# Kernel optimization log

Hardware: AMD Instinct MI355X
Metric: run time of the kernel (lower is better)

Reference implementation:

```python
import jax, jax.numpy as jnp
import numpy as np

B, S, D = 1, 2048, 4096
NH, NKV, HD = 32, 8, 128
N_REP = NH // NKV
NEG = -1e9


def setup_inputs() -> dict:
    key = jax.random.key(0)
    ks = jax.random.split(key, 8)
    x = jax.random.normal(ks[0], (B, S, D), dtype=jnp.float32)
    # rotary freqs (theta=10000), shape [S, HD//2]
    inv = 1.0 / (10000.0 ** (jnp.arange(0, HD, 2, dtype=jnp.float32) / HD))
    ang = jnp.arange(S, dtype=jnp.float32)[:, None] * inv[None, :]
    freqs_cos, freqs_sin = jnp.cos(ang), jnp.sin(ang)
    # causal mask [1,1,S,S]
    row = jnp.arange(S)[:, None]
    col = jnp.arange(S)[None, :]
    mask = jnp.where(col <= row, 0.0, NEG).astype(jnp.float32)[None, None]
    input_indexes = jnp.arange(S, dtype=jnp.int64)
    cache_k = jnp.zeros((B, S, NKV, HD), dtype=jnp.float32)
    cache_v = jnp.zeros((B, S, NKV, HD), dtype=jnp.float32)
    sc = 0.02
    wq = jax.random.normal(ks[1], (NH * HD, D), dtype=jnp.float32) * sc
    wk = jax.random.normal(ks[2], (NKV * HD, D), dtype=jnp.float32) * sc
    wv = jax.random.normal(ks[3], (NKV * HD, D), dtype=jnp.float32) * sc
    wo = jax.random.normal(ks[4], (NH * HD, D), dtype=jnp.float32).T * sc
    return {"x": x, "freqs_cos": freqs_cos, "freqs_sin": freqs_sin, "mask": mask,
            "input_indexes": input_indexes, "cache_k": cache_k, "cache_v": cache_v,
            "wq": wq, "wk": wk, "wv": wv, "wo": wo}


def _rope(t, cos, sin):
    # t: [B,S,H,HD]; treat last dim as HD//2 complex pairs (even=real, odd=imag)
    tr = t.reshape(*t.shape[:-1], HD // 2, 2)
    xr, xi = tr[..., 0], tr[..., 1]
    c = cos[None, :, None, :]  # [1,S,1,HD//2]
    s = sin[None, :, None, :]
    outr = xr * c - xi * s
    outi = xr * s + xi * c
    return jnp.stack([outr, outi], axis=-1).reshape(t.shape)


def reference(x, freqs_cos, freqs_sin, mask, input_indexes, cache_k, cache_v, wq, wk, wv, wo):
    bsz, seqlen = x.shape[0], x.shape[-2]
    xq = (x @ wq.T).reshape(bsz, seqlen, NH, HD)
    xk = (x @ wk.T).reshape(bsz, seqlen, NKV, HD)
    xv = (x @ wv.T).reshape(bsz, seqlen, NKV, HD)
    xq = _rope(xq, freqs_cos, freqs_sin)
    xk = _rope(xk, freqs_cos, freqs_sin)
    # KV-cache append (index_copy along seq dim)
    cache_k = cache_k.at[:, input_indexes].set(xk)
    cache_v = cache_v.at[:, input_indexes].set(xv)
    # GQA: repeat kv heads
    keys = jnp.repeat(cache_k, N_REP, axis=2)    # [B,S,NH,HD]
    values = jnp.repeat(cache_v, N_REP, axis=2)
    scores = jnp.einsum('bshd,bthd->bhst', xq, keys) / jnp.sqrt(jnp.float32(HD))
    scores = scores + mask
    probs = jax.nn.softmax(scores.astype(jnp.float32), axis=-1).astype(xq.dtype)
    out = jnp.einsum('bhst,bthd->bhsd', probs, values)
    out = out.transpose(0, 2, 1, 3).reshape(bsz, seqlen, -1)
    return (out @ wo.T, cache_k, cache_v)
```

## Files before the change

### kernel.cpp

```cpp
#include <hip/hip_runtime.h>
#include <cstdint>

#define S_LEN 2048
#define D_DIM 4096
#define NH_ 32
#define NKV_ 8
#define HD_ 128
#define GK 4096

typedef unsigned short u16;
typedef __attribute__((ext_vector_type(4))) float f32x4;
typedef __attribute__((ext_vector_type(8))) short bf16x8;
typedef __attribute__((ext_vector_type(4))) short s16x4;

__device__ __forceinline__ short f2bf(float f) {
  union { float f; unsigned int u; } v; v.f = f;
  unsigned int r = v.u + 0x7fffu + ((v.u >> 16) & 1u);
  return (short)(r >> 16);
}

__device__ __forceinline__ void glds16(const void* g, void* l) {
  __builtin_amdgcn_global_load_lds(
      (const __attribute__((address_space(1))) void*)g,
      (__attribute__((address_space(3))) void*)l, 16, 0, 0);
}

__global__ __launch_bounds__(256) void cvt_bf16(const float* __restrict__ src,
                                                u16* __restrict__ dst, int n8) {
  int i = blockIdx.x * 256 + threadIdx.x;
  if (i < n8) {
    float4 a = *(const float4*)&src[(size_t)i * 8];
    float4 b = *(const float4*)&src[(size_t)i * 8 + 4];
    bf16x8 o = { f2bf(a.x), f2bf(a.y), f2bf(a.z), f2bf(a.w),
                 f2bf(b.x), f2bf(b.y), f2bf(b.z), f2bf(b.w) };
    *(bf16x8*)&dst[(size_t)i * 8] = o;
  }
}

template <int MODE, int NI, int ATOMIC>
__global__ __launch_bounds__(512, 2) void gemm8(const u16* __restrict__ Amat,
                                                const u16* __restrict__ W,
                                                float* __restrict__ C,
                                                u16* __restrict__ qbf,
                                                u16* __restrict__ kbf,
                                                u16* __restrict__ vbf,
                                                float* __restrict__ cko,
                                                float* __restrict__ cvo,
                                                const float* __restrict__ fc,
                                                const float* __restrict__ fs,
                                                int N, int ktPer) {
  __shared__ __align__(16) u16 As[2][16384];
  __shared__ __align__(16) u16 Bs[2][NI * 4096];
  const int t = threadIdx.x;
  const int lane = t & 63;
  const int wave = t >> 6;
  const int wr = wave >> 2;
  const int wc = wave & 3;
  const int quad = lane >> 4;
  const int L = lane & 15;
  const int bm = blockIdx.y * 256;
  const int bn = blockIdx.x * (NI * 64);
  const int dr = lane >> 3;
  const int cb = lane & 7;
  const int cbs = cb ^ dr;
  const int kt0 = blockIdx.z * ktPer;
  const int ktN = kt0 + ktPer;

  auto stageA = [&](int tile) {
    u16* dst = &As[tile & 1][0];
    const int k0 = tile << 6;
#pragma unroll
    for (int c = 0; c < 4; ++c) {
      const int chunk = wave * 4 + c;
      const int row = chunk * 8 + dr;
      glds16(&Amat[(size_t)(bm + row) * GK + k0 + cbs * 8], &dst[chunk * 512]);
    }
  };
  auto stageB = [&](int tile) {
    u16* dst = &Bs[tile & 1][0];
    const int k0 = tile << 6;
#pragma unroll
    for (int c = 0; c < NI; ++c) {
      const int chunk = wave * NI + c;
      const int row = chunk * 8 + dr;
      glds16(&W[(size_t)(bn + row) * GK + k0 + cbs * 8], &dst[chunk * 512]);
    }
  };

  f32x4 acc[8][NI];
#pragma unroll
  for (int i = 0; i < 8; ++i)
#pragma unroll
    for (int j = 0; j < NI; ++j) { f32x4 z = {0.f, 0.f, 0.f, 0.f}; acc[i][j] = z; }

  stageB(kt0); stageA(kt0); stageB(kt0 + 1);
  if constexpr (NI == 3) asm volatile("s_waitcnt vmcnt(3)" ::: "memory");
  else                   asm volatile("s_waitcnt vmcnt(4)" ::: "memory");
  __builtin_amdgcn_s_barrier();
  __builtin_amdgcn_sched_barrier(0);

  bf16x8 af[4], bw[NI];
  const int arow = wr * 128;
  const int brow = wc * (NI * 16);

  for (int kt = kt0; kt < ktN; ++kt) {
    const u16* as = &As[kt & 1][0];
    const u16* bs = &Bs[kt & 1][0];
#pragma unroll
    for (int ph = 0; ph < 4; ++ph) {
      const int mh = ph & 1;
      const int s = ph >> 1;
#pragma unroll
      for (int i = 0; i < 4; ++i)
        af[i] = *(const bf16x8*)&as[(arow + mh * 64 + i * 16 + L) * 64 +
                                     (((s * 4 + quad) ^ (L & 7)) * 8)];
      if (ph == 0 || ph == 2) {
#pragma unroll
        for (int j = 0; j < NI; ++j)
          bw[j] = *(const bf16x8*)&bs[(brow + j * 16 + L) * 64 +
                                       (((s * 4 + quad) ^ (L & 7)) * 8)];
      }
      if (ph == 0 && kt + 1 < ktN) stageA(kt + 1);
      if (ph == 3 && kt + 2 < ktN) stageB(kt + 2);
      __builtin_amdgcn_s_barrier();
      asm volatile("s_waitcnt lgkmcnt(0)" ::: "memory");
      __builtin_amdgcn_sched_barrier(0);
      __builtin_amdgcn_s_setprio(1);
#pragma unroll
      for (int i = 0; i < 4; ++i)
#pragma unroll
        for (int j = 0; j < NI; ++j)
          acc[mh * 4 + i][j] = __builtin_amdgcn_mfma_f32_16x16x32_bf16(
              af[i], bw[j], acc[mh * 4 + i][j], 0, 0, 0);
      __builtin_amdgcn_s_setprio(0);
      if (ph == 3) {
        if (kt + 2 < ktN) {
          if constexpr (NI == 3) asm volatile("s_waitcnt vmcnt(3)" ::: "memory");
          else                   asm volatile("s_waitcnt vmcnt(4)" ::: "memory");
        } else {
          asm volatile("s_waitcnt vmcnt(0)" ::: "memory");
        }
      }
      __builtin_amdgcn_s_barrier();
      __builtin_amdgcn_sched_barrier(0);
    }
  }

  if (MODE == 0) {
#pragma unroll
    for (int mi = 0; mi < 8; ++mi) {
      int r0 = bm + wr * 128 + mi * 16 + quad * 4;
#pragma unroll
      for (int ni = 0; ni < NI; ++ni) {
        int c = bn + wc * (NI * 16) + ni * 16 + L;
#pragma unroll
        for (int r = 0; r < 4; ++r) {
          if (ATOMIC) unsafeAtomicAdd(&C[(size_t)(r0 + r) * N + c], acc[mi][ni][r]);
          else        C[(size_t)(r0 + r) * N + c] = acc[mi][ni][r];
        }
      }
    }
  } else {
    const float scale = 0.08838834764831845f;
#pragma unroll
    for (int mi = 0; mi < 8; ++mi) {
#pragma unroll
      for (int ni = 0; ni < NI; ++ni) {
        int c = bn + wc * (NI * 16) + ni * 16 + L;
#pragma unroll
        for (int r = 0; r < 4; ++r) {
          int srow = bm + wr * 128 + mi * 16 + 4 * quad + r;
          float v = acc[mi][ni][r];
          float partner = __shfl_xor(v, 1);
          if (c < 4096) {
            int p = (c >> 1) & 63;
            float co = fc[srow * 64 + p], si = fs[srow * 64 + p];
            float out = (c & 1) ? partner * si + v * co : v * co - partner * si;
            qbf[(size_t)srow * 4096 + c] = (u16)f2bf(out * scale);
          } else if (c < 5120) {
            int p = (c >> 1) & 63;
            float co = fc[srow * 64 + p], si = fs[srow * 64 + p];
            float out = (c & 1) ? partner * si + v * co : v * co - partner * si;
            int cc = c - 4096;
            cko[(size_t)srow * 1024 + cc] = out;
            kbf[(size_t)srow * 1024 + cc] = (u16)f2bf(out);
          } else {
            int cc = c - 5120;
            cvo[(size_t)srow * 1024 + cc] = v;
            vbf[(size_t)srow * 1024 + cc] = (u16)f2bf(v);
          }
        }
      }
    }
  }
}

__global__ __launch_bounds__(512, 2) void attn_bf(const u16* __restrict__ qbf,
                                                  const u16* __restrict__ kbf,
                                                  const u16* __restrict__ vbf,
                                                  u16* __restrict__ ao) {
  __shared__ __align__(16) u16 Ks[64 * 136];
  __shared__ __align__(16) u16 Vt[128 * 64];
  __shared__ __align__(16) u16 Ps[8 * 16 * 72];
  const int t = threadIdx.x;
  const int wave = t >> 6;
  const int lane = t & 63;
  const int Q4 = lane >> 4;
  const int L = lane & 15;
  const int h = blockIdx.y;
  const int qb = 15 - (int)blockIdx.x;
  const int kvh = h >> 2;
  const int qs0 = qb * 128;
  u16* Psw = &Ps[wave * 16 * 72];

  bf16x8 qf[4];
  {
    const u16* qbase = &qbf[(size_t)(qs0 + 16 * wave + L) * D_DIM + h * HD_ + 8 * Q4];
#pragma unroll
    for (int s = 0; s < 4; ++s) qf[s] = *(const bf16x8*)&qbase[32 * s];
  }

  f32x4 o[8];
#pragma unroll
  for (int jd = 0; jd < 8; ++jd) { f32x4 z = {0.f, 0.f, 0.f, 0.f}; o[jd] = z; }
  float mold[4] = {-1e30f, -1e30f, -1e30f, -1e30f};
  float lst[4] = {0.f, 0.f, 0.f, 0.f};

  const int NKT = 2 * qb + 2;
  for (int kt = 0; kt < NKT; ++kt) {
    __syncthreads();
    const u16* kb = &kbf[(size_t)(kt * 64) * (NKV_ * HD_) + kvh * HD_];
    const u16* vb = &vbf[(size_t)(kt * 64) * (NKV_ * HD_) + kvh * HD_];
#pragma unroll
    for (int p = 0; p < 2; ++p) {
      int u = t + 512 * p;
      int r = u >> 4, c8 = u & 15;
      *(bf16x8*)&Ks[r * 136 + c8 * 8] =
          *(const bf16x8*)&kb[(size_t)r * (NKV_ * HD_) + c8 * 8];
    }
#pragma unroll
    for (int p = 0; p < 2; ++p) {
      int u = t + 512 * p;
      int d = u & 127, bb = u >> 7;
      const u16* vsrc = &vb[(size_t)(bb * 8) * (NKV_ * HD_) + d];
      short vv[8];
#pragma unroll
      for (int j = 0; j < 8; ++j) vv[j] = (short)vsrc[(size_t)j * (NKV_ * HD_)];
      bf16x8 pk = { vv[0], vv[1], vv[2], vv[3], vv[4], vv[5], vv[6], vv[7] };
      *(bf16x8*)&Vt[d * 64 + ((bb + d) & 7) * 8] = pk;
    }
    __syncthreads();

    f32x4 sa[4];
#pragma unroll
    for (int jn = 0; jn < 4; ++jn) { f32x4 z = {0.f, 0.f, 0.f, 0.f}; sa[jn] = z; }
#pragma unroll
    for (int s = 0; s < 4; ++s) {
#pragma unroll
      for (int jn = 0; jn < 4; ++jn) {
        bf16x8 kf = *(const bf16x8*)&Ks[(16 * jn + L) * 136 + 32 * s + 8 * Q4];
        sa[jn] = __builtin_amdgcn_mfma_f32_16x16x32_bf16(qf[s], kf, sa[jn], 0, 0, 0);
      }
    }

    const int gq0 = qs0 + 16 * wave + 4 * Q4;
    const int gk0 = kt * 64 + L;
    float rmax[4];
#pragma unroll
    for (int r = 0; r < 4; ++r) {
#pragma unroll
      for (int jn = 0; jn < 4; ++jn)
        if (gk0 + 16 * jn > gq0 + r) sa[jn][r] = -1e30f;
      rmax[r] = fmaxf(fmaxf(sa[0][r], sa[1][r]), fmaxf(sa[2][r], sa[3][r]));
    }
#pragma unroll
    for (int m = 1; m < 16; m <<= 1) {
#pragma unroll
      for (int r = 0; r < 4; ++r) rmax[r] = fmaxf(rmax[r], __shfl_xor(rmax[r], m));
    }
    float p_[4][4], rsum[4], alpha[4];
#pragma unroll
    for (int r = 0; r < 4; ++r) {
      float mnew = fmaxf(mold[r], rmax[r]);
      alpha[r] = __expf(mold[r] - mnew);
#pragma unroll
      for (int jn = 0; jn < 4; ++jn) p_[jn][r] = __expf(sa[jn][r] - mnew);
      rsum[r] = (p_[0][r] + p_[1][r]) + (p_[2][r] + p_[3][r]);
      mold[r] = mnew;
    }
#pragma unroll
    for (int m = 1; m < 16; m <<= 1) {
#pragma unroll
      for (int r = 0; r < 4; ++r) rsum[r] += __shfl_xor(rsum[r], m);
    }
#pragma unroll
    for (int r = 0; r < 4; ++r) lst[r] = lst[r] * alpha[r] + rsum[r];
#pragma unroll
    for (int jd = 0; jd < 8; ++jd)
#pragma unroll
      for (int r = 0; r < 4; ++r) o[jd][r] *= alpha[r];

#pragma unroll
    for (int r = 0; r < 4; ++r)
#pragma unroll
      for (int jn = 0; jn < 4; ++jn)
        Psw[(4 * Q4 + r) * 72 + 16 * jn + L] = (u16)f2bf(p_[jn][r]);
    asm volatile("s_waitcnt lgkmcnt(0)" ::: "memory");

#pragma unroll
    for (int s2 = 0; s2 < 2; ++s2) {
      bf16x8 pa = *(const bf16x8*)&Psw[L * 72 + 32 * s2 + 8 * Q4];
#pragma unroll
      for (int jd = 0; jd < 8; ++jd) {
        bf16x8 vf = *(const bf16x8*)&Vt[(16 * jd + L) * 64 + ((4 * s2 + Q4 + L) & 7) * 8];
        o[jd] = __builtin_amdgcn_mfma_f32_16x16x32_bf16(pa, vf, o[jd], 0, 0, 0);
      }
    }
  }

  float inv[4];
#pragma unroll
  for (int r = 0; r < 4; ++r) inv[r] = 1.0f / lst[r];
#pragma unroll
  for (int r = 0; r < 4; ++r) {
    u16* dst = &ao[(size_t)(qs0 + 16 * wave + 4 * Q4 + r) * D_DIM + h * HD_ + L];
#pragma unroll
    for (int jd = 0; jd < 8; ++jd) dst[16 * jd] = (u16)f2bf(o[jd][r] * inv[r]);
  }
}

#define LDA 40
__global__ __launch_bounds__(256) void gemm_bt(const float* __restrict__ A,
                                               const float* __restrict__ W,
                                               float* __restrict__ C, int N) {
  __shared__ short As[128 * LDA];
  __shared__ short Bs[128 * LDA];
  const int t = threadIdx.x;
  const int lane = t & 63;
  const int wave = t >> 6;
  const int wm = (wave >> 1) * 64;
  const int wn = (wave & 1) * 64;
  const int quad = lane >> 4;
  const int l15 = lane & 15;
  const int bm = blockIdx.y * 128;
  const int bn = blockIdx.x * 128;
  f32x4 acc[4][4];
#pragma unroll
  for (int i = 0; i < 4; ++i)
#pragma unroll
    for (int j = 0; j < 4; ++j) { f32x4 z = {0.f, 0.f, 0.f, 0.f}; acc[i][j] = z; }
  for (int k0 = 0; k0 < GK; k0 += 32) {
    __syncthreads();
#pragma unroll
    for (int p = 0; p < 4; ++p) {
      int idx = p * 256 + t;
      int row = idx >> 3;
      int c4 = (idx & 7) * 4;
      const float4 av = *(const float4*)&A[(size_t)(bm + row) * GK + k0 + c4];
      const float4 wv = *(const float4*)&W[(size_t)(bn + row) * GK + k0 + c4];
      s16x4 a4 = { f2bf(av.x), f2bf(av.y), f2bf(av.z), f2bf(av.w) };
      s16x4 w4 = { f2bf(wv.x), f2bf(wv.y), f2bf(wv.z), f2bf(wv.w) };
      *(s16x4*)&As[row * LDA + c4] = a4;
      *(s16x4*)&Bs[row * LDA + c4] = w4;
    }
    __syncthreads();
    bf16x8 af[4], bfr[4];
#pragma unroll
    for (int i = 0; i < 4; ++i) {
      af[i]  = *(const bf16x8*)&As[(wm + i * 16 + l15) * LDA + quad * 8];
      bfr[i] = *(const bf16x8*)&Bs[(wn + i * 16 + l15) * LDA + quad * 8];
    }
#pragma unroll
    for (int i = 0; i < 4; ++i)
#pragma unroll
      for (int j = 0; j < 4; ++j)
        acc[i][j] = __builtin_amdgcn_mfma_f32_16x16x32_bf16(af[i], bfr[j], acc[i][j], 0, 0, 0);
  }
#pragma unroll
  for (int i = 0; i < 4; ++i) {
    int r0 = bm + wm + i * 16 + quad * 4;
#pragma unroll
    for (int j = 0; j < 4; ++j) {
      int c = bn + wn + j * 16 + l15;
#pragma unroll
      for (int r = 0; r < 4; ++r) C[(size_t)(r0 + r) * N + c] = acc[i][j][r];
    }
  }
}

__global__ __launch_bounds__(256) void rope_kernel(float* __restrict__ xq,
                                                   const float* __restrict__ xk,
                                                   float* __restrict__ cko,
                                                   const float* __restrict__ fc,
                                                   const float* __restrict__ fs) {
  int i = blockIdx.x * 256 + threadIdx.x;
  const int NQP = S_LEN * NH_ * (HD_ / 2);
  if (i < NQP) {
    int s = i >> 11; int rem = i & 2047; int p = rem & 63;
    float c = fc[s * 64 + p], sn = fs[s * 64 + p];
    float2 v = *(const float2*)&xq[(size_t)s * D_DIM + 2 * rem];
    *(float2*)&xq[(size_t)s * D_DIM + 2 * rem] =
        make_float2(v.x * c - v.y * sn, v.x * sn + v.y * c);
  } else {
    int j = i - NQP; int s = j >> 9; int rem = j & 511; int p = rem & 63;
    float c = fc[s * 64 + p], sn = fs[s * 64 + p];
    float2 v = *(const float2*)&xk[(size_t)s * (NKV_ * HD_) + 2 * rem];
    *(float2*)&cko[(size_t)s * (NKV_ * HD_) + 2 * rem] =
        make_float2(v.x * c - v.y * sn, v.x * sn + v.y * c);
  }
}

__global__ __launch_bounds__(256, 3) void attn_mfma(const float* __restrict__ xq,
                                                    const float* __restrict__ ck,
                                                    const float* __restrict__ cv,
                                                    float* __restrict__ outp) {
  __shared__ __align__(16) short Ks[64 * 136];
  __shared__ __align__(16) short Vt[128 * 64];
  __shared__ __align__(16) short Ps[4 * 16 * 72];
  const int t = threadIdx.x;
  const int wave = t >> 6;
  const int lane = t & 63;
  const int Q4 = lane >> 4;
  const int L = lane & 15;
  const int h = blockIdx.y;
  const int qb = 31 - (int)blockIdx.x;
  const int kvh = h >> 2;
  const int qs0 = qb * 64;
  const float scale = 0.08838834764831845f;
  short* Psw = &Ps[wave * 16 * 72];
  bf16x8 qf[4];
  {
    const float* qbase = &xq[(size_t)(qs0 + 16 * wave + L) * D_DIM + h * HD_ + 8 * Q4];
#pragma unroll
    for (int s = 0; s < 4; ++s) {
      float4 a = *(const float4*)&qbase[32 * s];
      float4 b = *(const float4*)&qbase[32 * s + 4];
      bf16x8 q8 = { f2bf(a.x * scale), f2bf(a.y * scale), f2bf(a.z * scale), f2bf(a.w * scale),
                    f2bf(b.x * scale), f2bf(b.y * scale), f2bf(b.z * scale), f2bf(b.w * scale) };
      qf[s] = q8;
    }
  }
  f32x4 o[8];
#pragma unroll
  for (int jd = 0; jd < 8; ++jd) { f32x4 z = {0.f, 0.f, 0.f, 0.f}; o[jd] = z; }
  float mold[4] = {-1e30f, -1e30f, -1e30f, -1e30f};
  float lst[4] = {0.f, 0.f, 0.f, 0.f};
  for (int kt = 0; kt <= qb; ++kt) {
    __syncthreads();
    const float* ckb = &ck[(size_t)(kt * 64) * (NKV_ * HD_) + kvh * HD_];
    const float* cvb = &cv[(size_t)(kt * 64) * (NKV_ * HD_) + kvh * HD_];
#pragma unroll
    for (int p = 0; p < 8; ++p) {
      int i = t + 256 * p;
      int r = i >> 5, c4 = (i & 31) * 4;
      float4 v = *(const float4*)&ckb[(size_t)r * (NKV_ * HD_) + c4];
      s16x4 k4 = { f2bf(v.x), f2bf(v.y), f2bf(v.z), f2bf(v.w) };
      *(s16x4*)&Ks[r * 136 + c4] = k4;
    }
#pragma unroll
    for (int p = 0; p < 4; ++p) {
      int u = t + 256 * p;
      int d = u & 127, bb = u >> 7;
      float vv[8];
#pragma unroll
      for (int j = 0; j < 8; ++j) vv[j] = cvb[(size_t)(bb * 8 + j) * (NKV_ * HD_) + d];
      bf16x8 pk = { f2bf(vv[0]), f2bf(vv[1]), f2bf(vv[2]), f2bf(vv[3]),
                    f2bf(vv[4]), f2bf(vv[5]), f2bf(vv[6]), f2bf(vv[7]) };
      *(bf16x8*)&Vt[d * 64 + ((bb + d) & 7) * 8] = pk;
    }
    __syncthreads();
    f32x4 sa[4];
#pragma unroll
    for (int jn = 0; jn < 4; ++jn) { f32x4 z = {0.f, 0.f, 0.f, 0.f}; sa[jn] = z; }
#pragma unroll
    for (int s = 0; s < 4; ++s) {
#pragma unroll
      for (int jn = 0; jn < 4; ++jn) {
        bf16x8 kf = *(const bf16x8*)&Ks[(16 * jn + L) * 136 + 32 * s + 8 * Q4];
        sa[jn] = __builtin_amdgcn_mfma_f32_16x16x32_bf16(qf[s], kf, sa[jn], 0, 0, 0);
      }
    }
    const int gq0 = qs0 + 16 * wave + 4 * Q4;
    const int gk0 = kt * 64 + L;
    float rmax[4];
#pragma unroll
    for (int r = 0; r < 4; ++r) {
#pragma unroll
      for (int jn = 0; jn < 4; ++jn)
        if (gk0 + 16 * jn > gq0 + r) sa[jn][r] = -1e30f;
      rmax[r] = fmaxf(fmaxf(sa[0][r], sa[1][r]), fmaxf(sa[2][r], sa[3][r]));
    }
#pragma unroll
    for (int m = 1; m < 16; m <<= 1) {
#pragma unroll
      for (int r = 0; r < 4; ++r) rmax[r] = fmaxf(rmax[r], __shfl_xor(rmax[r], m));
    }
    float p_[4][4], rsum[4], alpha[4];
#pragma unroll
    for (int r = 0; r < 4; ++r) {
      float mnew = fmaxf(mold[r], rmax[r]);
      alpha[r] = __expf(mold[r] - mnew);
#pragma unroll
      for (int jn = 0; jn < 4; ++jn) p_[jn][r] = __expf(sa[jn][r] - mnew);
      rsum[r] = (p_[0][r] + p_[1][r]) + (p_[2][r] + p_[3][r]);
      mold[r] = mnew;
    }
#pragma unroll
    for (int m = 1; m < 16; m <<= 1) {
#pragma unroll
      for (int r = 0; r < 4; ++r) rsum[r] += __shfl_xor(rsum[r], m);
    }
#pragma unroll
    for (int r = 0; r < 4; ++r) lst[r] = lst[r] * alpha[r] + rsum[r];
#pragma unroll
    for (int jd = 0; jd < 8; ++jd)
#pragma unroll
      for (int r = 0; r < 4; ++r) o[jd][r] *= alpha[r];
#pragma unroll
    for (int r = 0; r < 4; ++r)
#pragma unroll
      for (int jn = 0; jn < 4; ++jn)
        Psw[(4 * Q4 + r) * 72 + 16 * jn + L] = f2bf(p_[jn][r]);
    asm volatile("s_waitcnt lgkmcnt(0)" ::: "memory");
#pragma unroll
    for (int s2 = 0; s2 < 2; ++s2) {
      bf16x8 pa = *(const bf16x8*)&Psw[L * 72 + 32 * s2 + 8 * Q4];
#pragma unroll
      for (int jd = 0; jd < 8; ++jd) {
        bf16x8 vf = *(const bf16x8*)&Vt[(16 * jd + L) * 64 + ((4 * s2 + Q4 + L) & 7) * 8];
        o[jd] = __builtin_amdgcn_mfma_f32_16x16x32_bf16(pa, vf, o[jd], 0, 0, 0);
      }
    }
  }
  float inv[4];
#pragma unroll
  for (int r = 0; r < 4; ++r) inv[r] = 1.0f / lst[r];
#pragma unroll
  for (int r = 0; r < 4; ++r) {
    float* dst = &outp[(size_t)(qs0 + 16 * wave + 4 * Q4 + r) * D_DIM + h * HD_ + L];
#pragma unroll
    for (int jd = 0; jd < 8; ++jd) dst[16 * jd] = o[jd][r] * inv[r];
  }
}

extern "C" void kernel_launch(void* const* d_in, const int* in_sizes, int n_in,
                              void* d_out, int out_size, void* d_ws, size_t ws_size,
                              hipStream_t stream) {
  (void)in_sizes; (void)n_in; (void)out_size;
  const float* x  = (const float*)d_in[0];
  const float* fc = (const float*)d_in[1];
  const float* fs = (const float*)d_in[2];
  const float* wq = (const float*)d_in[7];
  const float* wk = (const float*)d_in[8];
  const float* wv = (const float*)d_in[9];
  const float* wo = (const float*)d_in[10];
  float* outp = (float*)d_out;
  float* ck = outp + (size_t)S_LEN * D_DIM;
  float* cv = ck + (size_t)S_LEN * NKV_ * HD_;

  if (ws_size >= 109051904ull) {
    u16* x_bf = (u16*)d_ws;
    u16* wqkv = x_bf + 8388608;
    u16* q_bf = wqkv + 25165824;
    u16* k_bf = q_bf + 8388608;
    u16* v_bf = k_bf + 2097152;
    u16* ao_bf = v_bf + 2097152;
    u16* wo_bf = wqkv;

    hipMemsetAsync(outp, 0, (size_t)S_LEN * D_DIM * sizeof(float), stream);

    cvt_bf16<<<4096, 256, 0, stream>>>(x, x_bf, 1048576);
    cvt_bf16<<<8192, 256, 0, stream>>>(wq, wqkv, 2097152);
    cvt_bf16<<<2048, 256, 0, stream>>>(wk, wqkv + 16777216, 524288);
    cvt_bf16<<<2048, 256, 0, stream>>>(wv, wqkv + 20971520, 524288);
    gemm8<1, 3, 0><<<dim3(32, 8, 1), 512, 0, stream>>>(
        x_bf, wqkv, nullptr, q_bf, k_bf, v_bf, ck, cv, fc, fs, 6144, 64);
    cvt_bf16<<<8192, 256, 0, stream>>>(wo, wo_bf, 2097152);
    attn_bf<<<dim3(16, 32), 512, 0, stream>>>(q_bf, k_bf, v_bf, ao_bf);
    gemm8<0, 4, 1><<<dim3(16, 8, 2), 512, 0, stream>>>(
        ao_bf, wo_bf, outp, nullptr, nullptr, nullptr, nullptr, nullptr,
        fc, fs, 4096, 32);
  } else {
    float* xq = (float*)d_ws;
    float* xk = xq + (size_t)S_LEN * D_DIM;
    dim3 blk(256);
    gemm_bt<<<dim3(32, 16), blk, 0, stream>>>(x, wq, xq, 4096);
    gemm_bt<<<dim3(8, 16),  blk, 0, stream>>>(x, wk, xk, 1024);
    gemm_bt<<<dim3(8, 16),  blk, 0, stream>>>(x, wv, cv, 1024);
    rope_kernel<<<20480, 256, 0, stream>>>(xq, xk, ck, fc, fs);
    attn_mfma<<<dim3(32, 32), 512 / 2, 0, stream>>>(xq, ck, cv, xq);
    gemm_bt<<<dim3(32, 16), blk, 0, stream>>>(xq, wo, outp, 4096);
  }
}
```

Before: 631.1 us.

## Register-prefetch next K/V tile in attention and rebalance causal block order

The attention kernel now loads the next K/V tile from global memory into registers while the current tile is computed, then stores it to shared memory after a barrier. This hides global load latency behind MFMA work, at the cost of extra registers. The 2D grid becomes a 1D grid of 512 blocks: the first 256 take even query blocks in increasing order and the last 256 take odd blocks in decreasing order, spreading causal work more evenly. The P scratch row pitch also changes from 72 to 68 to alter LDS bank mapping.

```diff
diff --git a/kernel.cpp b/kernel.cpp
--- a/kernel.cpp
+++ b/kernel.cpp
@@ -195,23 +195,27 @@
   }
 }
 
+#define PSP 68
 __global__ __launch_bounds__(512, 2) void attn_bf(const u16* __restrict__ qbf,
                                                   const u16* __restrict__ kbf,
                                                   const u16* __restrict__ vbf,
                                                   u16* __restrict__ ao) {
   __shared__ __align__(16) u16 Ks[64 * 136];
   __shared__ __align__(16) u16 Vt[128 * 64];
-  __shared__ __align__(16) u16 Ps[8 * 16 * 72];
+  __shared__ __align__(16) u16 Ps[8 * 16 * PSP];
   const int t = threadIdx.x;
   const int wave = t >> 6;
   const int lane = t & 63;
   const int Q4 = lane >> 4;
   const int L = lane & 15;
-  const int h = blockIdx.y;
-  const int qb = 15 - (int)blockIdx.x;
+  const int id = blockIdx.x;
+  const int slot = id & 255;
+  const int h = slot >> 3;
+  const int k8 = slot & 7;
+  const int qb = (id < 256) ? (2 * k8) : (15 - 2 * k8);
   const int kvh = h >> 2;
   const int qs0 = qb * 128;
-  u16* Psw = &Ps[wave * 16 * 72];
+  u16* Psw = &Ps[wave * 16 * PSP];
 
   bf16x8 qf[4];
   {
@@ -227,16 +231,15 @@
   float lst[4] = {0.f, 0.f, 0.f, 0.f};
 
   const int NKT = 2 * qb + 2;
-  for (int kt = 0; kt < NKT; ++kt) {
-    __syncthreads();
+
+  auto loadKV = [&](int kt, bf16x8 kr[2], bf16x8 vr[2]) {
     const u16* kb = &kbf[(size_t)(kt * 64) * (NKV_ * HD_) + kvh * HD_];
     const u16* vb = &vbf[(size_t)(kt * 64) * (NKV_ * HD_) + kvh * HD_];
 #pragma unroll
     for (int p = 0; p < 2; ++p) {
       int u = t + 512 * p;
       int r = u >> 4, c8 = u & 15;
-      *(bf16x8*)&Ks[r * 136 + c8 * 8] =
-          *(const bf16x8*)&kb[(size_t)r * (NKV_ * HD_) + c8 * 8];
+      kr[p] = *(const bf16x8*)&kb[(size_t)r * (NKV_ * HD_) + c8 * 8];
     }
 #pragma unroll
     for (int p = 0; p < 2; ++p) {
@@ -247,10 +250,25 @@
 #pragma unroll
       for (int j = 0; j < 8; ++j) vv[j] = (short)vsrc[(size_t)j * (NKV_ * HD_)];
       bf16x8 pk = { vv[0], vv[1], vv[2], vv[3], vv[4], vv[5], vv[6], vv[7] };
-      *(bf16x8*)&Vt[d * 64 + ((bb + d) & 7) * 8] = pk;
-    }
-    __syncthreads();
-
+      vr[p] = pk;
+    }
+  };
+  auto storeKV = [&](bf16x8 kr[2], bf16x8 vr[2]) {
+#pragma unroll
+    for (int p = 0; p < 2; ++p) {
+      int u = t + 512 * p;
+      int r = u >> 4, c8 = u & 15;
+      *(bf16x8*)&Ks[r * 136 + c8 * 8] = kr[p];
+    }
+#pragma unroll
+    for (int p = 0; p < 2; ++p) {
+      int u = t + 512 * p;
+      int d = u & 127, bb = u >> 7;
+      *(bf16x8*)&Vt[d * 64 + ((bb + d) & 7) * 8] = vr[p];
+    }
+  };
+
+  auto computeTile = [&](int kt) {
     f32x4 sa[4];
 #pragma unroll
     for (int jn = 0; jn < 4; ++jn) { f32x4 z = {0.f, 0.f, 0.f, 0.f}; sa[jn] = z; }
@@ -304,18 +322,33 @@
     for (int r = 0; r < 4; ++r)
 #pragma unroll
       for (int jn = 0; jn < 4; ++jn)
-        Psw[(4 * Q4 + r) * 72 + 16 * jn + L] = (u16)f2bf(p_[jn][r]);
+        Psw[(4 * Q4 + r) * PSP + 16 * jn + L] = (u16)f2bf(p_[jn][r]);
     asm volatile("s_waitcnt lgkmcnt(0)" ::: "memory");
 
 #pragma unroll
     for (int s2 = 0; s2 < 2; ++s2) {
-      bf16x8 pa = *(const bf16x8*)&Psw[L * 72 + 32 * s2 + 8 * Q4];
+      bf16x8 pa = *(const bf16x8*)&Psw[L * PSP + 32 * s2 + 8 * Q4];
 #pragma unroll
       for (int jd = 0; jd < 8; ++jd) {
         bf16x8 vf = *(const bf16x8*)&Vt[(16 * jd + L) * 64 + ((4 * s2 + Q4 + L) & 7) * 8];
         o[jd] = __builtin_amdgcn_mfma_f32_16x16x32_bf16(pa, vf, o[jd], 0, 0, 0);
       }
     }
+  };
+
+  bf16x8 krA[2], vrA[2], krB[2], vrB[2];
+  loadKV(0, krA, vrA);
+  for (int kt = 0; kt < NKT; kt += 2) {
+    __syncthreads();
+    storeKV(krA, vrA);
+    loadKV(kt + 1, krB, vrB);
+    __syncthreads();
+    computeTile(kt);
+    __syncthreads();
+    storeKV(krB, vrB);
+    if (kt + 2 < NKT) loadKV(kt + 2, krA, vrA);
+    __syncthreads();
+    computeTile(kt + 1);
   }
 
   float inv[4];
@@ -576,7 +609,7 @@
     gemm8<1, 3, 0><<<dim3(32, 8, 1), 512, 0, stream>>>(
         x_bf, wqkv, nullptr, q_bf, k_bf, v_bf, ck, cv, fc, fs, 6144, 64);
     cvt_bf16<<<8192, 256, 0, stream>>>(wo, wo_bf, 2097152);
-    attn_bf<<<dim3(16, 32), 512, 0, stream>>>(q_bf, k_bf, v_bf, ao_bf);
+    attn_bf<<<dim3(512), 512, 0, stream>>>(q_bf, k_bf, v_bf, ao_bf);
     gemm8<0, 4, 1><<<dim3(16, 8, 2), 512, 0, stream>>>(
         ao_bf, wo_bf, outp, nullptr, nullptr, nullptr, nullptr, nullptr,
         fc, fs, 4096, 32);
```

After: 593.2 us. 1.06x faster.
